# Optimization experiments

Hardware: AMD Instinct MI355X
Metric: run time of the kernel (lower is better)

Reference implementation:

```python
import jax, jax.numpy as jnp
import numpy as np
from jax import lax

M1, M2 = 16, 16  # retained Fourier modes per spatial dim


def _spectral_conv(x, w1, w2):
    # x: [B, C, H, W] real; w1/w2: [C, C, M1, M2, 2] (re, im)
    B, C, H, W = x.shape
    xf = jnp.fft.rfft2(x, norm='ortho')            # [B, C, H, W//2+1] complex
    w1c = w1[..., 0] + 1j * w1[..., 1]
    w2c = w2[..., 0] + 1j * w2[..., 1]
    top = jnp.einsum('bixy,ioxy->boxy', xf[:, :, :M1, :M2], w1c)
    bot = jnp.einsum('bixy,ioxy->boxy', xf[:, :, -M1:, :M2], w2c)
    of = jnp.zeros((B, C, H, W // 2 + 1), dtype=xf.dtype)
    of = of.at[:, :, :M1, :M2].set(top).at[:, :, -M1:, :M2].set(bot)
    return jnp.fft.irfft2(of, s=(H, W), norm='ortho')


def _fno_block(x, w1, w2, skip_w):
    # spectral conv + linear (1x1 conv, no bias) skip
    return _spectral_conv(x, w1, w2) + jnp.einsum('bixy,io->boxy', x, skip_w)


def setup_inputs() -> dict:
    key = jax.random.key(0)
    ks = jax.random.split(key, 6)
    B, T, C, H, W = 4, 8, 64, 64, 64
    scale = 1.0 / (C * C)
    return {
        'x': jax.random.normal(ks[0], (B, T, C, H, W), dtype=jnp.float32),
        'sw1': jax.random.normal(ks[1], (6, C, C, M1, M2, 2), dtype=jnp.float32) * scale,
        'sw2': jax.random.normal(ks[2], (6, C, C, M1, M2, 2), dtype=jnp.float32) * scale,
        'skw': jax.random.normal(ks[3], (6, C, C), dtype=jnp.float32) * 0.02,
        'gate_b': jax.random.normal(ks[4], (3,), dtype=jnp.float32),
        'bias_h': jax.random.normal(ks[5], (1,), dtype=jnp.float32),
    }


def reference(x, sw1, sw2, skw, gate_b, bias_h):
    B, T, C, H, W = x.shape

    def f(i, inp):
        return _fno_block(inp, sw1[i], sw2[i], skw[i])

    def cell(xt, h):
        z = jax.nn.sigmoid(f(0, xt) + f(1, h) + gate_b[0])
        r = jax.nn.sigmoid(f(2, xt) + f(3, h) + gate_b[1])
        h_hat = jax.nn.selu(f(4, xt) + f(5, r * h) + gate_b[2])
        return (1.0 - z) * h + z * h_hat

    def step(h, xt):
        h = cell(xt, h)
        return h, None

    h0 = jnp.full((B, C, H, W), bias_h[0], dtype=x.dtype)
    h_final, _ = lax.scan(step, h0, jnp.moveaxis(x, 1, 0))  # scan over T
    return h_final  # return_sequences=False -> final hidden state [B, C, H, W]
```

## Files before the change

### kernel.cpp

```cpp
#include <hip/hip_runtime.h>

#define BB_ 4
#define TT_ 8
#define CC_ 64
#define HW 4096
#define UMAP 1024
#define STEP 0.09817477042468103f

#define OFF_UXALL 0
#define OFF_UH    (OFF_UXALL + TT_*256*UMAP)
#define OFF_URH   (OFF_UH + 256*UMAP)
#define OFF_SX    (OFF_URH + 256*UMAP)
#define OFF_SPART (OFF_SX + 3*TT_*256*UMAP)
#define OFF_H     (OFF_SPART + 2*8*256*UMAP)
#define OFF_Z     (OFF_H + BB_*CC_*HW)
#define OFF_RH    (OFF_Z + BB_*CC_*HW)
#define OFF_PH    (OFF_RH + BB_*CC_*HW)

__global__ __launch_bounds__(256) void k_init(float* __restrict__ hb,
                                              float* __restrict__ Uh,
                                              const float* __restrict__ bias_h) {
    float v = bias_h[0];
    int blk = blockIdx.x;
    if (blk < 1024) {
        int idx = (blk * 256 + threadIdx.x) * 4;
        *(float4*)(hb + idx) = make_float4(v, v, v, v);
    } else {
        int map = blk - 1024;
        float4 z = make_float4(0.f, 0.f, 0.f, 0.f);
        if (threadIdx.x == 0) z.x = 64.f * v;
        *(float4*)(Uh + (size_t)map * UMAP + threadIdx.x * 4) = z;
    }
}

__device__ __forceinline__ void dft_stages(const float* __restrict__ su,
                                           float* __restrict__ FxR, float* __restrict__ FxI,
                                           float* __restrict__ dst) {
    int tid = threadIdx.x;
    int kx = tid & 15, yb = tid >> 4;
    float stc, sts;
    __sincosf(-STEP * (float)kx, &sts, &stc);
    float wr = 1.f, wi = 0.f;
    float aR[4] = {0, 0, 0, 0}, aI[4] = {0, 0, 0, 0};
    for (int x = 0; x < 64; x++) {
        #pragma unroll
        for (int j = 0; j < 4; j++) {
            float v = su[(yb + 16 * j) * 65 + x];
            aR[j] = fmaf(v, wr, aR[j]);
            aI[j] = fmaf(v, wi, aI[j]);
        }
        float t = wr * stc - wi * sts;
        wi = wr * sts + wi * stc;
        wr = t;
    }
    #pragma unroll
    for (int j = 0; j < 4; j++) {
        FxR[(yb + 16 * j) * 16 + kx] = aR[j];
        FxI[(yb + 16 * j) * 16 + kx] = aI[j];
    }
    __syncthreads();
    int kb = tid >> 4;
    float c0, s0, c1, s1;
    __sincosf(-STEP * (float)kb, &s0, &c0);
    __sincosf(-STEP * (float)(kb + 48), &s1, &c1);
    float w0r = 1, w0i = 0, w1r = 1, w1i = 0;
    float A0r = 0, A0i = 0, A1r = 0, A1i = 0;
    for (int y = 0; y < 64; y++) {
        float Fr = FxR[y * 16 + kx], Fi = FxI[y * 16 + kx];
        A0r = fmaf(Fr, w0r, A0r); A0r = fmaf(-Fi, w0i, A0r);
        A0i = fmaf(Fr, w0i, A0i); A0i = fmaf(Fi, w0r, A0i);
        A1r = fmaf(Fr, w1r, A1r); A1r = fmaf(-Fi, w1i, A1r);
        A1i = fmaf(Fr, w1i, A1i); A1i = fmaf(Fi, w1r, A1i);
        float t0 = w0r * c0 - w0i * s0; w0i = w0r * s0 + w0i * c0; w0r = t0;
        float t1 = w1r * c1 - w1i * s1; w1i = w1r * s1 + w1i * c1; w1r = t1;
    }
    const float sc = 1.f / 64.f;
    float2* d2 = (float2*)dst;
    d2[kb * 16 + kx]        = make_float2(A0r * sc, A0i * sc);
    d2[(kb + 16) * 16 + kx] = make_float2(A1r * sc, A1i * sc);
}

__global__ __launch_bounds__(256) void k_dft_x(const float* __restrict__ x,
                                               float* __restrict__ Uxall) {
    __shared__ float su[64 * 65];
    __shared__ float FxR[1024], FxI[1024];
    int blk = blockIdx.x;
    int t = blk >> 8, map = blk & 255;
    int b = map >> 6, c = map & 63;
    const float* src = x + (((size_t)b * TT_ + t) * CC_ + c) * HW;
    int tid = threadIdx.x;
    #pragma unroll
    for (int k = 0; k < 4; k++) {
        int off = k * 1024 + tid * 4;
        float4 v = *(const float4*)(src + off);
        int y = off >> 6, xx = off & 63;
        su[y * 65 + xx + 0] = v.x; su[y * 65 + xx + 1] = v.y;
        su[y * 65 + xx + 2] = v.z; su[y * 65 + xx + 3] = v.w;
    }
    __syncthreads();
    dft_stages(su, FxR, FxI, Uxall + ((size_t)t * 256 + map) * UMAP);
}

__device__ __forceinline__ void mix_load(const float2* __restrict__ W2,
                                         const float2* __restrict__ U2, int i,
                                         float2 w[4], float2 u[4]) {
    const float2* wp = W2 + (size_t)i * 16384;
    const float2* up = U2 + (size_t)i * 512;
    w[0] = wp[0]; w[1] = wp[256]; w[2] = wp[512]; w[3] = wp[768];
    u[0] = up[0]; u[1] = up[32768]; u[2] = up[65536]; u[3] = up[98304];
}

__device__ __forceinline__ void mix_fma(const float2 w[4], const float2 u[4],
                                        float aR[4][4], float aI[4][4]) {
    #pragma unroll
    for (int oo = 0; oo < 4; oo++)
        #pragma unroll
        for (int bb = 0; bb < 4; bb++) {
            aR[oo][bb] = fmaf(u[bb].x, w[oo].x, aR[oo][bb]);
            aR[oo][bb] = fmaf(-u[bb].y, w[oo].y, aR[oo][bb]);
            aI[oo][bb] = fmaf(u[bb].x, w[oo].y, aI[oo][bb]);
            aI[oo][bb] = fmaf(u[bb].y, w[oo].x, aI[oo][bb]);
        }
}

__device__ __forceinline__ void mix_accum(const float2* __restrict__ W2,
                                          const float2* __restrict__ U2,
                                          int niter, float aR[4][4], float aI[4][4])
{
    float2 wA[4], uA[4], wB[4], uB[4], wN[4], uN[4];
    mix_load(W2, U2, 0, wA, uA);
    mix_load(W2, U2, 1, wB, uB);
    for (int i = 0; i + 2 < niter; i += 2) {
        mix_load(W2, U2, i + 2, wN, uN);
        mix_fma(wA, uA, aR, aI);
        #pragma unroll
        for (int k = 0; k < 4; k++) { wA[k] = wN[k]; uA[k] = uN[k]; }
        mix_load(W2, U2, i + 3, wN, uN);
        mix_fma(wB, uB, aR, aI);
        #pragma unroll
        for (int k = 0; k < 4; k++) { wB[k] = wN[k]; uB[k] = uN[k]; }
    }
    mix_fma(wA, uA, aR, aI);
    mix_fma(wB, uB, aR, aI);
}

__global__ __launch_bounds__(256) void k_mix_x(
    const float* __restrict__ Uxall,
    const float* __restrict__ sw1, const float* __restrict__ sw2,
    float* __restrict__ Sx)
{
    int blk = blockIdx.x;
    int og = blk & 15;
    int half = (blk >> 4) & 1;
    int t = (blk >> 5) & 7;
    int li = blk >> 8;
    int l = li * 2;
    int m = threadIdx.x;
    int o0 = og * 4;
    const float2* wt = (const float2*)(half ? sw2 : sw1);
    const float2* W2 = wt + (((size_t)l * 64) * 64 + o0) * 256 + m;
    const float2* U2 = (const float2*)Uxall + ((size_t)t * 256) * 512 + half * 256 + m;
    float aR[4][4], aI[4][4];
    #pragma unroll
    for (int oo = 0; oo < 4; oo++)
        #pragma unroll
        for (int b = 0; b < 4; b++) { aR[oo][b] = 0.f; aI[oo][b] = 0.f; }
    mix_accum(W2, U2, 64, aR, aI);
    float2* S2 = (float2*)Sx;
    #pragma unroll
    for (int oo = 0; oo < 4; oo++)
        #pragma unroll
        for (int b = 0; b < 4; b++)
            S2[((size_t)(li * 8 + t) * 256 + b * 64 + o0 + oo) * 512 + half * 256 + m]
                = make_float2(aR[oo][b], aI[oo][b]);
}

__device__ __forceinline__ void mix_body_h(int blk, int l0, int l1,
    const float* __restrict__ U,
    const float* __restrict__ sw1, const float* __restrict__ sw2,
    float* __restrict__ Spart)
{
    int og = blk & 15;
    int ic = (blk >> 4) & 7;
    int half = (blk >> 7) & 1;
    int g = (blk >> 8) & 1;
    int m = threadIdx.x;
    int o0 = og * 4, ib = ic * 8;
    int l = g ? l1 : l0;
    const float2* wt = (const float2*)(half ? sw2 : sw1);
    const float2* W2 = wt + (((size_t)l * 64 + ib) * 64 + o0) * 256 + m;
    const float2* U2 = (const float2*)U + (size_t)ib * 512 + half * 256 + m;
    float aR[4][4], aI[4][4];
    #pragma unroll
    for (int oo = 0; oo < 4; oo++)
        #pragma unroll
        for (int b = 0; b < 4; b++) { aR[oo][b] = 0.f; aI[oo][b] = 0.f; }
    mix_accum(W2, U2, 8, aR, aI);
    float2* S2 = (float2*)Spart;
    #pragma unroll
    for (int oo = 0; oo < 4; oo++)
        #pragma unroll
        for (int b = 0; b < 4; b++)
            S2[((size_t)(g * 8 + ic) * 256 + b * 64 + o0 + oo) * 512 + half * 256 + m]
                = make_float2(aR[oo][b], aI[oo][b]);
}

__device__ __forceinline__ void skip_v2(int r, float* __restrict__ sW,
    const float* __restrict__ uA, long long bsA,
    const float* __restrict__ uB, long long bsB,
    const float* __restrict__ skw, int lA, int lB, float gb,
    float* __restrict__ out)
{
    int pxt = r & 15, ot = (r >> 4) & 3, b = r >> 6;
    int tid = threadIdx.x;
    int px = pxt * 256 + tid;
    int o0 = ot * 16;
    for (int n = 0; n < 8; n++) {
        int idx = n * 256 + tid;
        int p = idx >> 10, i = (idx >> 4) & 63, k = idx & 15;
        sW[idx] = skw[(p ? lB : lA) * 4096 + i * 64 + o0 + k];
    }
    __syncthreads();
    float acc[16];
    #pragma unroll
    for (int k = 0; k < 16; k++) acc[k] = 0.f;
    const float* pa = uA + (long long)b * bsA + px;
    const float* pb = uB + (long long)b * bsB + px;
    const float4* sA4 = (const float4*)sW;
    const float4* sB4 = (const float4*)(sW + 1024);
    #pragma unroll 4
    for (int i = 0; i < 64; i++) {
        float ua = pa[(size_t)i * HW];
        float ub = pb[(size_t)i * HW];
        #pragma unroll
        for (int q = 0; q < 4; q++) {
            float4 wa = sA4[i * 4 + q];
            float4 wb = sB4[i * 4 + q];
            acc[4 * q + 0] = fmaf(ua, wa.x, acc[4 * q + 0]);
            acc[4 * q + 0] = fmaf(ub, wb.x, acc[4 * q + 0]);
            acc[4 * q + 1] = fmaf(ua, wa.y, acc[4 * q + 1]);
            acc[4 * q + 1] = fmaf(ub, wb.y, acc[4 * q + 1]);
            acc[4 * q + 2] = fmaf(ua, wa.z, acc[4 * q + 2]);
            acc[4 * q + 2] = fmaf(ub, wb.z, acc[4 * q + 2]);
            acc[4 * q + 3] = fmaf(ua, wa.w, acc[4 * q + 3]);
            acc[4 * q + 3] = fmaf(ub, wb.w, acc[4 * q + 3]);
        }
    }
    float* op = out + ((long long)b * 64 + o0) * HW + px;
    #pragma unroll
    for (int k = 0; k < 16; k++) op[(size_t)k * HW] = acc[k] + gb;
}

__global__ __launch_bounds__(256) void k_front_zr(
    const float* __restrict__ Uh,
    const float* __restrict__ xt, const float* __restrict__ hb,
    const float* __restrict__ sw1, const float* __restrict__ sw2,
    const float* __restrict__ skw, const float* __restrict__ gate_b,
    float* __restrict__ Spart, float* __restrict__ zb, float* __restrict__ rhb)
{
    __shared__ float smem[2048];
    int blk = blockIdx.x;
    if (blk < 512) {
        mix_body_h(blk, 1, 3, Uh, sw1, sw2, Spart);
    } else {
        int r = blk - 512;
        int g = r >> 8;
        skip_v2(r & 255, smem,
                xt, (long long)TT_ * CC_ * HW, hb, (long long)CC_ * HW,
                skw, g ? 2 : 0, g ? 3 : 1, gate_b[g], g ? rhb : zb);
    }
}

__global__ __launch_bounds__(256) void k_front_h(
    const float* __restrict__ Urh,
    const float* __restrict__ xt, const float* __restrict__ rhb,
    const float* __restrict__ sw1, const float* __restrict__ sw2,
    const float* __restrict__ skw, const float* __restrict__ gate_b,
    float* __restrict__ Spart, float* __restrict__ phb)
{
    __shared__ float smem[2048];
    int blk = blockIdx.x;
    if (blk < 256) {
        mix_body_h(blk, 5, 5, Urh, sw1, sw2, Spart);
    } else {
        int r = blk - 256;
        skip_v2(r, smem,
                xt, (long long)TT_ * CC_ * HW, rhb, (long long)CC_ * HW,
                skw, 4, 5, gate_b[2], phb);
    }
}

__device__ __forceinline__ void idft_stage1(const float* __restrict__ SR,
                                            const float* __restrict__ SI,
                                            float* __restrict__ GR, float* __restrict__ GI)
{
    int tid = threadIdx.x;
    int kx = tid & 15, yb = tid >> 4;
    #pragma unroll
    for (int j = 0; j < 4; j++) {
        int y = yb + 16 * j;
        float stc, sts;
        __sincosf(STEP * (float)y, &sts, &stc);
        float ar = 0.f, ai = 0.f;
        float wr = 1.f, wi = 0.f;
        for (int k = 0; k < 16; k++) {
            float sr_ = SR[k * 16 + kx], si_ = SI[k * 16 + kx];
            ar = fmaf(sr_, wr, ar); ar = fmaf(-si_, wi, ar);
            ai = fmaf(sr_, wi, ai); ai = fmaf(si_, wr, ai);
            float t = wr * stc - wi * sts; wi = wr * sts + wi * stc; wr = t;
        }
        int q = (3 * y) & 3;
        float w2r = (q == 0) ? 1.f : ((q == 2) ? -1.f : 0.f);
        float w2i = (q == 1) ? 1.f : ((q == 3) ? -1.f : 0.f);
        for (int k = 16; k < 32; k++) {
            float sr_ = SR[k * 16 + kx], si_ = SI[k * 16 + kx];
            ar = fmaf(sr_, w2r, ar); ar = fmaf(-si_, w2i, ar);
            ai = fmaf(sr_, w2i, ai); ai = fmaf(si_, w2r, ai);
            float t = w2r * stc - w2i * sts; w2i = w2r * sts + w2i * stc; w2r = t;
        }
        GR[y * 16 + kx] = ar;
        GI[y * 16 + kx] = ai;
    }
}

__global__ __launch_bounds__(256) void k_back_zr(
    const float* __restrict__ Spart, const float* __restrict__ Sx, int t,
    float* __restrict__ zb, float* __restrict__ rhb,
    const float* __restrict__ hb, float* __restrict__ Urh)
{
    __shared__ float smem[6208];
    float* SR = smem;
    float* SI = smem + 512;
    float* GR = smem + 1024;
    float* GI = smem + 2048;
    int g = blockIdx.x >> 8;
    int map = blockIdx.x & 255;
    int tid = threadIdx.x;
    {
        float4 v = ((const float4*)Sx)[((size_t)(g * 8 + t) * 256 + map) * 256 + tid];
        float sxr = v.x, sxi = v.y, syr = v.z, syi = v.w;
        const float4* base = (const float4*)Spart;
        #pragma unroll
        for (int ic = 0; ic < 8; ic++) {
            float4 p = base[((size_t)(g * 8 + ic) * 256 + map) * 256 + tid];
            sxr += p.x; sxi += p.y; syr += p.z; syi += p.w;
        }
        SR[2 * tid] = sxr; SI[2 * tid] = sxi;
        SR[2 * tid + 1] = syr; SI[2 * tid + 1] = syi;
    }
    __syncthreads();
    idft_stage1(SR, SI, GR, GI);
    __syncthreads();
    int x = tid & 63, ybase = tid >> 6;
    float cx, sx;
    __sincosf(STEP * (float)x, &sx, &cx);
    size_t mo = (size_t)map * HW;
    float rhv[16];
    #pragma unroll
    for (int j = 0; j < 16; j++) {
        int y = ybase + 4 * j;
        float acc = GR[y * 16];
        float wr = cx, wi = sx;
        #pragma unroll
        for (int k = 1; k < 16; k++) {
            acc = fmaf(2.f * GR[y * 16 + k], wr, acc);
            acc = fmaf(-2.f * GI[y * 16 + k], wi, acc);
            float t2 = wr * cx - wi * sx; wi = wr * sx + wi * cx; wr = t2;
        }
        float val = acc * (1.f / 64.f);
        int idx = y * 64 + x;
        if (g == 0) {
            float pre = val + zb[mo + idx];
            zb[mo + idx] = 1.f / (1.f + __expf(-pre));
        } else {
            float pre = val + rhb[mo + idx];
            float rr = 1.f / (1.f + __expf(-pre));
            float rh = rr * hb[mo + idx];
            rhb[mo + idx] = rh;
            rhv[j] = rh;
        }
    }
    if (g == 0) return;
    __syncthreads();
    float* su = smem;
    #pragma unroll
    for (int j = 0; j < 16; j++) {
        int y = ybase + 4 * j;
        su[y * 65 + x] = rhv[j];
    }
    __syncthreads();
    dft_stages(su, smem + 4160, smem + 5184, Urh + (size_t)map * UMAP);
}

__global__ __launch_bounds__(256) void k_back_h(
    const float* __restrict__ Spart, const float* __restrict__ Sx, int t,
    const float* __restrict__ zb, const float* __restrict__ phb,
    float* __restrict__ hb, float* __restrict__ Uh)
{
    __shared__ float smem[6208];
    float* SR = smem;
    float* SI = smem + 512;
    float* GR = smem + 1024;
    float* GI = smem + 2048;
    int map = blockIdx.x & 255;
    int tid = threadIdx.x;
    {
        float4 v = ((const float4*)Sx)[((size_t)(2 * 8 + t) * 256 + map) * 256 + tid];
        float sxr = v.x, sxi = v.y, syr = v.z, syi = v.w;
        const float4* base = (const float4*)Spart;
        #pragma unroll
        for (int ic = 0; ic < 8; ic++) {
            float4 p = base[((size_t)ic * 256 + map) * 256 + tid];
            sxr += p.x; sxi += p.y; syr += p.z; syi += p.w;
        }
        SR[2 * tid] = sxr; SI[2 * tid] = sxi;
        SR[2 * tid + 1] = syr; SI[2 * tid + 1] = syi;
    }
    __syncthreads();
    idft_stage1(SR, SI, GR, GI);
    __syncthreads();
    int x = tid & 63, ybase = tid >> 6;
    float cx, sx;
    __sincosf(STEP * (float)x, &sx, &cx);
    size_t mo = (size_t)map * HW;
    float hv[16];
    #pragma unroll
    for (int j = 0; j < 16; j++) {
        int y = ybase + 4 * j;
        float acc = GR[y * 16];
        float wr = cx, wi = sx;
        #pragma unroll
        for (int k = 1; k < 16; k++) {
            acc = fmaf(2.f * GR[y * 16 + k], wr, acc);
            acc = fmaf(-2.f * GI[y * 16 + k], wi, acc);
            float t2 = wr * cx - wi * sx; wi = wr * sx + wi * cx; wr = t2;
        }
        float val = acc * (1.f / 64.f);
        int idx = y * 64 + x;
        float pre = val + phb[mo + idx];
        float hh = (pre > 0.f) ? 1.0507009873554805f * pre
                               : 1.7580993408473766f * (__expf(pre) - 1.f);
        float z = zb[mo + idx];
        float hn = fmaf(z, hh - hb[mo + idx], hb[mo + idx]);
        hb[mo + idx] = hn;
        hv[j] = hn;
    }
    __syncthreads();
    float* su = smem;
    #pragma unroll
    for (int j = 0; j < 16; j++) {
        int y = ybase + 4 * j;
        su[y * 65 + x] = hv[j];
    }
    __syncthreads();
    dft_stages(su, smem + 4160, smem + 5184, Uh + (size_t)map * UMAP);
}

extern "C" void kernel_launch(void* const* d_in, const int* in_sizes, int n_in,
                              void* d_out, int out_size, void* d_ws, size_t ws_size,
                              hipStream_t stream)
{
    (void)in_sizes; (void)n_in; (void)out_size; (void)ws_size;
    const float* x   = (const float*)d_in[0];
    const float* sw1 = (const float*)d_in[1];
    const float* sw2 = (const float*)d_in[2];
    const float* skw = (const float*)d_in[3];
    const float* gb  = (const float*)d_in[4];
    const float* bh  = (const float*)d_in[5];
    float* ws    = (float*)d_ws;
    float* Uxall = ws + OFF_UXALL;
    float* Uh    = ws + OFF_UH;
    float* Urh   = ws + OFF_URH;
    float* Sx    = ws + OFF_SX;
    float* Sp    = ws + OFF_SPART;
    float* hb    = ws + OFF_H;
    float* zb    = ws + OFF_Z;
    float* rhb   = ws + OFF_RH;
    float* phb   = ws + OFF_PH;

    k_init<<<1280, 256, 0, stream>>>(hb, Uh, bh);
    k_dft_x<<<2048, 256, 0, stream>>>(x, Uxall);
    k_mix_x<<<768, 256, 0, stream>>>(Uxall, sw1, sw2, Sx);
    for (int t = 0; t < TT_; t++) {
        const float* xt = x + (size_t)t * CC_ * HW;
        k_front_zr<<<1024, 256, 0, stream>>>(Uh, xt, hb, sw1, sw2, skw, gb,
                                             Sp, zb, rhb);
        k_back_zr<<<512, 256, 0, stream>>>(Sp, Sx, t, zb, rhb, hb, Urh);
        k_front_h<<<512, 256, 0, stream>>>(Urh, xt, rhb, sw1, sw2, skw, gb,
                                           Sp, phb);
        k_back_h<<<256, 256, 0, stream>>>(Sp, Sx, t, zb, phb, hb, Uh);
    }
    hipMemcpyAsync(d_out, hb, (size_t)BB_ * CC_ * HW * sizeof(float),
                   hipMemcpyDeviceToDevice, stream);
}
```

Baseline: 873.0 us.

## Register-tile skip GEMM 4x4 and deepen spectral-mix load pipeline

The 1x1 skip conv is rewritten so each thread computes a 4-output by 4-pixel register tile with float4 loads and stores. Each block now covers 32 output channels and 128 pixels and stages a larger weight slice in shared memory. The old scheme gave each thread 16 outputs for a single pixel using scalar input loads. The x-path spectral mix also gets a 4-deep software-pipelined accumulation loop to hide more load latency. The cost is more registers, which may reduce occupancy, and doubled shared memory per block.

```diff
diff --git a/kernel.cpp b/kernel.cpp
--- a/kernel.cpp
+++ b/kernel.cpp
@@ -144,6 +144,39 @@
     mix_fma(wB, uB, aR, aI);
 }
 
+__device__ __forceinline__ void mix_accum4(const float2* __restrict__ W2,
+                                           const float2* __restrict__ U2,
+                                           float aR[4][4], float aI[4][4])
+{
+    float2 w0[4], u0[4], w1[4], u1[4], w2[4], u2[4], w3[4], u3[4], wN[4], uN[4];
+    mix_load(W2, U2, 0, w0, u0);
+    mix_load(W2, U2, 1, w1, u1);
+    mix_load(W2, U2, 2, w2, u2);
+    mix_load(W2, U2, 3, w3, u3);
+    for (int i = 0; i < 60; i += 4) {
+        mix_load(W2, U2, i + 4, wN, uN);
+        mix_fma(w0, u0, aR, aI);
+        #pragma unroll
+        for (int k = 0; k < 4; k++) { w0[k] = wN[k]; u0[k] = uN[k]; }
+        mix_load(W2, U2, i + 5, wN, uN);
+        mix_fma(w1, u1, aR, aI);
+        #pragma unroll
+        for (int k = 0; k < 4; k++) { w1[k] = wN[k]; u1[k] = uN[k]; }
+        mix_load(W2, U2, i + 6, wN, uN);
+        mix_fma(w2, u2, aR, aI);
+        #pragma unroll
+        for (int k = 0; k < 4; k++) { w2[k] = wN[k]; u2[k] = uN[k]; }
+        mix_load(W2, U2, i + 7, wN, uN);
+        mix_fma(w3, u3, aR, aI);
+        #pragma unroll
+        for (int k = 0; k < 4; k++) { w3[k] = wN[k]; u3[k] = uN[k]; }
+    }
+    mix_fma(w0, u0, aR, aI);
+    mix_fma(w1, u1, aR, aI);
+    mix_fma(w2, u2, aR, aI);
+    mix_fma(w3, u3, aR, aI);
+}
+
 __global__ __launch_bounds__(256) void k_mix_x(
     const float* __restrict__ Uxall,
     const float* __restrict__ sw1, const float* __restrict__ sw2,
@@ -165,7 +198,7 @@
     for (int oo = 0; oo < 4; oo++)
         #pragma unroll
         for (int b = 0; b < 4; b++) { aR[oo][b] = 0.f; aI[oo][b] = 0.f; }
-    mix_accum(W2, U2, 64, aR, aI);
+    mix_accum4(W2, U2, aR, aI);
     float2* S2 = (float2*)Sx;
     #pragma unroll
     for (int oo = 0; oo < 4; oo++)
@@ -205,50 +238,59 @@
                 = make_float2(aR[oo][b], aI[oo][b]);
 }
 
-__device__ __forceinline__ void skip_v2(int r, float* __restrict__ sW,
+__device__ __forceinline__ void fma16(const float4 w, const float4 u, float acc[4][4]) {
+    acc[0][0] = fmaf(u.x, w.x, acc[0][0]); acc[0][1] = fmaf(u.y, w.x, acc[0][1]);
+    acc[0][2] = fmaf(u.z, w.x, acc[0][2]); acc[0][3] = fmaf(u.w, w.x, acc[0][3]);
+    acc[1][0] = fmaf(u.x, w.y, acc[1][0]); acc[1][1] = fmaf(u.y, w.y, acc[1][1]);
+    acc[1][2] = fmaf(u.z, w.y, acc[1][2]); acc[1][3] = fmaf(u.w, w.y, acc[1][3]);
+    acc[2][0] = fmaf(u.x, w.z, acc[2][0]); acc[2][1] = fmaf(u.y, w.z, acc[2][1]);
+    acc[2][2] = fmaf(u.z, w.z, acc[2][2]); acc[2][3] = fmaf(u.w, w.z, acc[2][3]);
+    acc[3][0] = fmaf(u.x, w.w, acc[3][0]); acc[3][1] = fmaf(u.y, w.w, acc[3][1]);
+    acc[3][2] = fmaf(u.z, w.w, acc[3][2]); acc[3][3] = fmaf(u.w, w.w, acc[3][3]);
+}
+
+__device__ __forceinline__ void skip_gemm(int rr, float* __restrict__ sW,
     const float* __restrict__ uA, long long bsA,
     const float* __restrict__ uB, long long bsB,
     const float* __restrict__ skw, int lA, int lB, float gb,
     float* __restrict__ out)
 {
-    int pxt = r & 15, ot = (r >> 4) & 3, b = r >> 6;
+    int pxc = rr & 31, oh = (rr >> 5) & 1, b = rr >> 6;
     int tid = threadIdx.x;
-    int px = pxt * 256 + tid;
-    int o0 = ot * 16;
-    for (int n = 0; n < 8; n++) {
-        int idx = n * 256 + tid;
-        int p = idx >> 10, i = (idx >> 4) & 63, k = idx & 15;
-        sW[idx] = skw[(p ? lB : lA) * 4096 + i * 64 + o0 + k];
-    }
-    __syncthreads();
-    float acc[16];
-    #pragma unroll
-    for (int k = 0; k < 16; k++) acc[k] = 0.f;
-    const float* pa = uA + (long long)b * bsA + px;
-    const float* pb = uB + (long long)b * bsB + px;
-    const float4* sA4 = (const float4*)sW;
-    const float4* sB4 = (const float4*)(sW + 1024);
+    int ot = tid & 7, pt = tid >> 3;
+    #pragma unroll
+    for (int n = 0; n < 4; n++) {
+        int idx = n * 1024 + tid * 4;
+        int k = idx >> 5, oc = idx & 31;
+        int p = k >> 6, i = k & 63;
+        *(float4*)(sW + idx) =
+            *(const float4*)(skw + (p ? lB : lA) * 4096 + i * 64 + oh * 32 + oc);
+    }
+    __syncthreads();
+    float acc[4][4];
+    #pragma unroll
+    for (int oo = 0; oo < 4; oo++)
+        #pragma unroll
+        for (int q = 0; q < 4; q++) acc[oo][q] = 0.f;
+    const float* pa = uA + (long long)b * bsA + pxc * 128 + pt * 4;
+    const float* pb = uB + (long long)b * bsB + pxc * 128 + pt * 4;
+    const float4* sW4 = (const float4*)sW;
     #pragma unroll 4
     for (int i = 0; i < 64; i++) {
-        float ua = pa[(size_t)i * HW];
-        float ub = pb[(size_t)i * HW];
-        #pragma unroll
-        for (int q = 0; q < 4; q++) {
-            float4 wa = sA4[i * 4 + q];
-            float4 wb = sB4[i * 4 + q];
-            acc[4 * q + 0] = fmaf(ua, wa.x, acc[4 * q + 0]);
-            acc[4 * q + 0] = fmaf(ub, wb.x, acc[4 * q + 0]);
-            acc[4 * q + 1] = fmaf(ua, wa.y, acc[4 * q + 1]);
-            acc[4 * q + 1] = fmaf(ub, wb.y, acc[4 * q + 1]);
-            acc[4 * q + 2] = fmaf(ua, wa.z, acc[4 * q + 2]);
-            acc[4 * q + 2] = fmaf(ub, wb.z, acc[4 * q + 2]);
-            acc[4 * q + 3] = fmaf(ua, wa.w, acc[4 * q + 3]);
-            acc[4 * q + 3] = fmaf(ub, wb.w, acc[4 * q + 3]);
-        }
-    }
-    float* op = out + ((long long)b * 64 + o0) * HW + px;
-    #pragma unroll
-    for (int k = 0; k < 16; k++) op[(size_t)k * HW] = acc[k] + gb;
+        float4 ua = *(const float4*)(pa + (size_t)i * HW);
+        float4 wa = sW4[i * 8 + ot];
+        fma16(wa, ua, acc);
+        float4 ub = *(const float4*)(pb + (size_t)i * HW);
+        float4 wb = sW4[(64 + i) * 8 + ot];
+        fma16(wb, ub, acc);
+    }
+    float* op = out + ((long long)(b * 64 + oh * 32 + ot * 4)) * HW + pxc * 128 + pt * 4;
+    #pragma unroll
+    for (int oo = 0; oo < 4; oo++) {
+        float4 r = make_float4(acc[oo][0] + gb, acc[oo][1] + gb,
+                               acc[oo][2] + gb, acc[oo][3] + gb);
+        *(float4*)(op + (size_t)oo * HW) = r;
+    }
 }
 
 __global__ __launch_bounds__(256) void k_front_zr(
@@ -258,16 +300,16 @@
     const float* __restrict__ skw, const float* __restrict__ gate_b,
     float* __restrict__ Spart, float* __restrict__ zb, float* __restrict__ rhb)
 {
-    __shared__ float smem[2048];
+    __shared__ float smem[4096];
     int blk = blockIdx.x;
     if (blk < 512) {
         mix_body_h(blk, 1, 3, Uh, sw1, sw2, Spart);
     } else {
         int r = blk - 512;
         int g = r >> 8;
-        skip_v2(r & 255, smem,
-                xt, (long long)TT_ * CC_ * HW, hb, (long long)CC_ * HW,
-                skw, g ? 2 : 0, g ? 3 : 1, gate_b[g], g ? rhb : zb);
+        skip_gemm(r & 255, smem,
+                  xt, (long long)TT_ * CC_ * HW, hb, (long long)CC_ * HW,
+                  skw, g ? 2 : 0, g ? 3 : 1, gate_b[g], g ? rhb : zb);
     }
 }
 
@@ -278,15 +320,15 @@
     const float* __restrict__ skw, const float* __restrict__ gate_b,
     float* __restrict__ Spart, float* __restrict__ phb)
 {
-    __shared__ float smem[2048];
+    __shared__ float smem[4096];
     int blk = blockIdx.x;
     if (blk < 256) {
         mix_body_h(blk, 5, 5, Urh, sw1, sw2, Spart);
     } else {
         int r = blk - 256;
-        skip_v2(r, smem,
-                xt, (long long)TT_ * CC_ * HW, rhb, (long long)CC_ * HW,
-                skw, 4, 5, gate_b[2], phb);
+        skip_gemm(r, smem,
+                  xt, (long long)TT_ * CC_ * HW, rhb, (long long)CC_ * HW,
+                  skw, 4, 5, gate_b[2], phb);
     }
 }
 
```

After: 851.8 us. 2.4% less time.
